# Kernel optimization log

Measured on AMD Instinct MI355X. Metric: run time of the kernel, lower is better.

## Reference

```python
import jax, jax.numpy as jnp
import numpy as np
from functools import partial

H = 51  # hidden size hard-coded in the module
B = 1024
T = 1024


def setup_inputs() -> dict:
    key = jax.random.key(0)
    ks = jax.random.split(key, 12)
    scale = 1.0 / np.sqrt(H)
    p = lambda k, shape: (jax.random.normal(k, shape, dtype=jnp.float32) * scale)
    return {
        "input": jax.random.normal(ks[0], (B, T), dtype=jnp.float32),
        # layer 1: LSTMCell(1, 51)
        "W_ih1": p(ks[1], (4 * H, 1)),
        "W_hh1": p(ks[2], (4 * H, H)),
        "b_ih1": p(ks[3], (4 * H,)),
        "b_hh1": p(ks[4], (4 * H,)),
        # layer 2: LSTMCell(51, 51)
        "W_ih2": p(ks[5], (4 * H, H)),
        "W_hh2": p(ks[6], (4 * H, H)),
        "b_ih2": p(ks[7], (4 * H,)),
        "b_hh2": p(ks[8], (4 * H,)),
        # Linear(51, 1)
        "W_lin": p(ks[9], (1, H)),
        "b_lin": p(ks[10], (1,)),
    }


def _lstm_cell(x, h, c, W_ih, W_hh, b_ih, b_hh):
    # PyTorch LSTMCell gate order: i, f, g, o
    gates = x @ W_ih.T + h @ W_hh.T + b_ih + b_hh  # [B, 4H]
    i, f, g, o = jnp.split(gates, 4, axis=-1)
    i = jax.nn.sigmoid(i)
    f = jax.nn.sigmoid(f)
    g = jnp.tanh(g)
    o = jax.nn.sigmoid(o)
    c_new = f * c + i * g
    h_new = o * jnp.tanh(c_new)
    return h_new, c_new


def reference(input, W_ih1, W_hh1, b_ih1, b_hh1, W_ih2, W_hh2, b_ih2, b_hh2, W_lin, b_lin):
    Bv = input.shape[0]
    dt = input.dtype
    init = (
        jnp.zeros((Bv, H), dt),  # h1
        jnp.zeros((Bv, H), dt),  # c1
        jnp.zeros((Bv, H), dt),  # h2
        jnp.zeros((Bv, H), dt),  # c2
    )

    def step(carry, x_t):  # x_t: [B, 1]
        h1, c1, h2, c2 = carry
        h1, c1 = _lstm_cell(x_t, h1, c1, W_ih1, W_hh1, b_ih1, b_hh1)
        h2, c2 = _lstm_cell(h1, h2, c2, W_ih2, W_hh2, b_ih2, b_hh2)
        y = h2 @ W_lin.T + b_lin  # [B, 1]
        return (h1, c1, h2, c2), y[:, 0]

    xs = input.T[:, :, None]  # [T, B, 1]
    _, ys = jax.lax.scan(step, init, xs)  # ys: [T, B]
    return ys.T  # [B, T]
```

## Files before the change

### kernel.cpp

```cpp
#include <hip/hip_runtime.h>


#define H     51
#define NROW  204
#define TLEN  1024
#define BPB   16
#define NTHR  896
#define NBLK  64
#define KPAD  88

#define LOG2E  1.442695041f
#define LOG2E2 2.885390082f

typedef __attribute__((ext_vector_type(8))) _Float16 half8;
typedef __attribute__((ext_vector_type(4))) float f4;

__device__ __forceinline__ float frcp(float x) { return __builtin_amdgcn_rcpf(x); }
#if __has_builtin(__builtin_amdgcn_exp2f)
__device__ __forceinline__ float ex2(float x) { return __builtin_amdgcn_exp2f(x); }
#else
__device__ __forceinline__ float ex2(float x) { return __expf(x * 0.6931471806f); }
#endif

__device__ __forceinline__ int posu(int u) {
    return (u & ~7) | ((u & 3) << 1) | ((u >> 2) & 1);
}
__device__ __forceinline__ int ipos(int p) {
    return (p & ~7) | ((p & 1) << 2) | ((p >> 1) & 3);
}

__device__ __forceinline__ half8 lds8h(const _Float16* p) {
    return *(const half8*)__builtin_assume_aligned(p, 16);
}

__device__ __forceinline__ void block_sync_lds() {
    asm volatile("s_waitcnt lgkmcnt(0)\n\ts_barrier" ::: "memory");
}

#define MFMA(ACC, A, B) \
    ACC = __builtin_amdgcn_mfma_f32_16x16x32_f16((A), (B), (ACC), 0, 0, 0)

__device__ __forceinline__ half8 load_wfrag(const float* __restrict__ W,
                                            int tile, int kt, int q, int mcol)
{
    half8 hf;
    const int prow = tile * 16 + mcol;
    const float sc = ((prow & 3) == 2) ? LOG2E2 : LOG2E;
#pragma unroll
    for (int j = 0; j < 8; ++j) {
        const int kk = ipos(kt * 32 + q * 8 + j);
        float v = 0.0f;
        if (prow < NROW && kk < H) {
            const int srow = (prow & 3) * H + (prow >> 2);
            v = W[srow * H + kk];
        }
        hf[j] = (_Float16)(v * sc);
    }
    return hf;
}

__device__ __forceinline__ float cell(float a_i, float a_f, float b_g,
                                      float d_o, float* c)
{
    const float e_i = ex2(-a_i);
    const float e_f = ex2(-a_f);
    const float Eg  = ex2(b_g);
    const float f   = frcp(1.0f + e_f);
    const float ig  = (Eg - 1.0f) * frcp((1.0f + e_i) * (Eg + 1.0f));
    const float cn  = fmaf(f, *c, ig);
    *c = cn;
    const float Ec  = ex2(cn * LOG2E2);
    const float e_o = ex2(-d_o);
    return (Ec - 1.0f) * frcp((Ec + 1.0f) * (1.0f + e_o));
}

__global__
__attribute__((amdgpu_flat_work_group_size(NTHR, NTHR), amdgpu_waves_per_eu(4, 4)))
void lstm2_kernel(const float* __restrict__ input,
                  const float* __restrict__ W_ih1, const float* __restrict__ W_hh1,
                  const float* __restrict__ b_ih1, const float* __restrict__ b_hh1,
                  const float* __restrict__ W_ih2, const float* __restrict__ W_hh2,
                  const float* __restrict__ b_ih2, const float* __restrict__ b_hh2,
                  const float* __restrict__ W_lin, const float* __restrict__ b_lin,
                  float* __restrict__ out)
{
    const int tid  = threadIdx.x;
    const int w    = tid >> 6;
    const int lane = tid & 63;
    const int q    = lane >> 4;
    const int mcol = lane & 15;
    const int b0   = blockIdx.x * BPB;

    const bool tile_wave = (w < 13);
    const bool y_wave    = (w == 13);

    __shared__ __align__(16) _Float16 hb[2][2][BPB][KPAD];

    {
        _Float16* hz = &hb[0][0][0][0];
        for (int i = tid; i < 2 * 2 * BPB * KPAD; i += NTHR) hz[i] = (_Float16)0.0f;
    }

    half8 A1[2], Ai[2], Ah[2];
    f4 bb1, bb2, wxv;
    float c1 = 0.0f, c2 = 0.0f;
    const int t = w;
    const int u = 4 * t + q;
    const int wpos = posu(u);

    if (tile_wave) {
#pragma unroll
        for (int kt = 0; kt < 2; ++kt) {
            A1[kt] = load_wfrag(W_hh1, t, kt, q, mcol);
            Ai[kt] = load_wfrag(W_ih2, t, kt, q, mcol);
            Ah[kt] = load_wfrag(W_hh2, t, kt, q, mcol);
        }
#pragma unroll
        for (int j = 0; j < 4; ++j) {
            const bool v = (u < H);
            const float sc = (j == 2) ? LOG2E2 : LOG2E;
            bb1[j] = v ? sc * (b_ih1[j * H + u] + b_hh1[j * H + u]) : 0.0f;
            bb2[j] = v ? sc * (b_ih2[j * H + u] + b_hh2[j * H + u]) : 0.0f;
            wxv[j] = v ? sc * W_ih1[j * H + u] : 0.0f;
        }
    }

    float wl[16];
    if (y_wave) {
#pragma unroll
        for (int i = 0; i < 16; ++i) {
            const int r = ipos(q * 16 + i);
            wl[i] = (r < H) ? W_lin[r] : 0.0f;
        }
    }
    const float blin = b_lin[0];

    float xcur = input[(size_t)(b0 + mcol) * TLEN + 0];

    __syncthreads();

#define STEP(KK, RB, WB, L2EN, YEN)                                            \
do {                                                                           \
    const int k_  = (KK);                                                      \
    const int kn_ = (k_ + 1 < TLEN) ? (k_ + 1) : (TLEN - 1);                   \
    const float xnext_ = input[(size_t)(b0 + mcol) * TLEN + kn_];              \
    if (tile_wave) {                                                           \
        half8 B1a = lds8h(&hb[RB][0][mcol][q * 8]);                            \
        half8 B1b = lds8h(&hb[RB][0][mcol][32 + q * 8]);                       \
        f4 g1;                                                                 \
        g1[0] = fmaf(wxv[0], xcur, bb1[0]);                                    \
        g1[1] = fmaf(wxv[1], xcur, bb1[1]);                                    \
        g1[2] = fmaf(wxv[2], xcur, bb1[2]);                                    \
        g1[3] = fmaf(wxv[3], xcur, bb1[3]);                                    \
        MFMA(g1, A1[0], B1a);  MFMA(g1, A1[1], B1b);                           \
                                                         \
        const float h1n = cell(g1[0], g1[1], g1[2], g1[3], &c1);               \
        hb[WB][0][mcol][wpos] = (_Float16)h1n;                                 \
        if (L2EN) {                                                            \
            half8 B2a = lds8h(&hb[RB][1][mcol][q * 8]);                        \
            half8 B2b = lds8h(&hb[RB][1][mcol][32 + q * 8]);                   \
            f4 g2 = bb2;                                                       \
            MFMA(g2, Ai[0], B1a);  MFMA(g2, Ai[1], B1b);                       \
            MFMA(g2, Ah[0], B2a);  MFMA(g2, Ah[1], B2b);                       \
                                                       \
            const float h2n = cell(g2[0], g2[1], g2[2], g2[3], &c2);           \
            hb[WB][1][mcol][wpos] = (_Float16)h2n;                             \
        }                                                                      \
    } else if (y_wave && (YEN)) {                                              \
               \
        half8 y0 = lds8h(&hb[RB][1][mcol][q * 16]);                            \
        half8 y1 = lds8h(&hb[RB][1][mcol][q * 16 + 8]);                        \
        float yp = 0.0f;                                                       \
        _Pragma("unroll")                                                      \
        for (int i = 0; i < 8; ++i) {                                          \
            yp += wl[i]     * (float)y0[i];                                    \
            yp += wl[i + 8] * (float)y1[i];                                    \
        }                                                                      \
        yp += __shfl_xor(yp, 16);                                              \
        yp += __shfl_xor(yp, 32);                                              \
        if (q == 0) out[(size_t)(b0 + mcol) * TLEN + (k_ - 2)] = yp + blin;    \
    }                                                                          \
    block_sync_lds();                                                          \
    xcur = xnext_;                                                             \
} while (0)

    STEP(0, 1, 0, 0, 0);
    STEP(1, 0, 1, 1, 0);
    for (int k = 2; k < TLEN; k += 2) {
        STEP(k, 1, 0, 1, 1);
        STEP(k + 1, 0, 1, 1, 1);
    }
    STEP(TLEN, 1, 0, 1, 1);
#undef STEP

    if (y_wave) {
        half8 y0 = lds8h(&hb[0][1][mcol][q * 16]);
        half8 y1 = lds8h(&hb[0][1][mcol][q * 16 + 8]);
        float yp = 0.0f;
#pragma unroll
        for (int i = 0; i < 8; ++i) {
            yp += wl[i]     * (float)y0[i];
            yp += wl[i + 8] * (float)y1[i];
        }
        yp += __shfl_xor(yp, 16);
        yp += __shfl_xor(yp, 32);
        if (q == 0) out[(size_t)(b0 + mcol) * TLEN + (TLEN - 1)] = yp + blin;
    }
}

extern "C" void kernel_launch(void* const* d_in, const int* in_sizes, int n_in,
                              void* d_out, int out_size, void* d_ws, size_t ws_size,
                              hipStream_t stream)
{
    const float* input = (const float*)d_in[0];
    const float* W_ih1 = (const float*)d_in[1];
    const float* W_hh1 = (const float*)d_in[2];
    const float* b_ih1 = (const float*)d_in[3];
    const float* b_hh1 = (const float*)d_in[4];
    const float* W_ih2 = (const float*)d_in[5];
    const float* W_hh2 = (const float*)d_in[6];
    const float* b_ih2 = (const float*)d_in[7];
    const float* b_hh2 = (const float*)d_in[8];
    const float* W_lin = (const float*)d_in[9];
    const float* b_lin = (const float*)d_in[10];

    float* out = (float*)d_out;

    hipLaunchKernelGGL(lstm2_kernel, dim3(NBLK), dim3(NTHR), 0, stream,
                       input, W_ih1, W_hh1, b_ih1, b_hh1,
                       W_ih2, W_hh2, b_ih2, b_hh2, W_lin, b_lin,
                       out);
}
```

Baseline: 772.0 us.

## Split LSTM layers across wave groups and pipeline layer 2 one step behind

Waves are re-partitioned so 7 waves compute layer 1 and 7 compute layer 2, with each wave owning two gate tiles. Layer 2 uses h1 prefetched into registers from the previous step, so the two layers run concurrently on different timesteps instead of serially inside one step. The separate output wave is removed and the linear projection is folded into a layer-2 wave that reuses the h2 fragments it already loaded. The change adds a four-deep h1 ring buffer, more registers per wave, a longer pipeline prologue and epilogue, and more complex index bookkeeping that could hide correctness errors.

```diff
diff --git a/kernel.cpp b/kernel.cpp
--- a/kernel.cpp
+++ b/kernel.cpp
@@ -91,116 +91,154 @@
     const int mcol = lane & 15;
     const int b0   = blockIdx.x * BPB;
 
-    const bool tile_wave = (w < 13);
-    const bool y_wave    = (w == 13);
-
-    __shared__ __align__(16) _Float16 hb[2][2][BPB][KPAD];
+    const bool isL1 = (w < 7);
+    const int  tw   = isL1 ? w : (w - 7);
+
+    __shared__ __align__(16) _Float16 h1r[4][BPB][KPAD];
+    __shared__ __align__(16) _Float16 h2r[2][BPB][KPAD];
 
     {
-        _Float16* hz = &hb[0][0][0][0];
-        for (int i = tid; i < 2 * 2 * BPB * KPAD; i += NTHR) hz[i] = (_Float16)0.0f;
-    }
-
-    half8 A1[2], Ai[2], Ah[2];
-    f4 bb1, bb2, wxv;
-    float c1 = 0.0f, c2 = 0.0f;
-    const int t = w;
-    const int u = 4 * t + q;
-    const int wpos = posu(u);
-
-    if (tile_wave) {
+        _Float16* p1 = &h1r[0][0][0];
+        for (int i = tid; i < 4 * BPB * KPAD; i += NTHR) p1[i] = (_Float16)0.0f;
+        _Float16* p2 = &h2r[0][0][0];
+        for (int i = tid; i < 2 * BPB * KPAD; i += NTHR) p2[i] = (_Float16)0.0f;
+    }
+
+    half8 Wa[2][2], Wb[2][2];
+    f4 bbv[2], wxv[2];
+    float cc[2] = {0.0f, 0.0f};
+    int wp[2];
+    const int tt[2] = {tw, 7 + tw};
+#pragma unroll
+    for (int s = 0; s < 2; ++s) {
+        const int t = tt[s];
+        const int u = 4 * t + q;
+        wp[s] = posu(u);
 #pragma unroll
         for (int kt = 0; kt < 2; ++kt) {
-            A1[kt] = load_wfrag(W_hh1, t, kt, q, mcol);
-            Ai[kt] = load_wfrag(W_ih2, t, kt, q, mcol);
-            Ah[kt] = load_wfrag(W_hh2, t, kt, q, mcol);
+            if (isL1) {
+                Wa[s][kt] = load_wfrag(W_hh1, t, kt, q, mcol);
+            } else {
+                Wa[s][kt] = load_wfrag(W_ih2, t, kt, q, mcol);
+                Wb[s][kt] = load_wfrag(W_hh2, t, kt, q, mcol);
+            }
         }
 #pragma unroll
         for (int j = 0; j < 4; ++j) {
-            const bool v = (u < H);
+            const bool v = (t < 13) && (u < H);
             const float sc = (j == 2) ? LOG2E2 : LOG2E;
-            bb1[j] = v ? sc * (b_ih1[j * H + u] + b_hh1[j * H + u]) : 0.0f;
-            bb2[j] = v ? sc * (b_ih2[j * H + u] + b_hh2[j * H + u]) : 0.0f;
-            wxv[j] = v ? sc * W_ih1[j * H + u] : 0.0f;
-        }
-    }
-
-    float wl[16];
-    if (y_wave) {
-#pragma unroll
-        for (int i = 0; i < 16; ++i) {
-            const int r = ipos(q * 16 + i);
-            wl[i] = (r < H) ? W_lin[r] : 0.0f;
+            if (isL1) {
+                bbv[s][j] = v ? sc * (b_ih1[j * H + u] + b_hh1[j * H + u]) : 0.0f;
+                wxv[s][j] = v ? sc * W_ih1[j * H + u] : 0.0f;
+            } else {
+                bbv[s][j] = v ? sc * (b_ih2[j * H + u] + b_hh2[j * H + u]) : 0.0f;
+                wxv[s][j] = 0.0f;
+            }
+        }
+    }
+
+    float wl_a[8], wl_b[8];
+    if (w == 7) {
+#pragma unroll
+        for (int j = 0; j < 8; ++j) {
+            const int ra = ipos(q * 8 + j);
+            const int rb = ipos(32 + q * 8 + j);
+            wl_a[j] = (ra < H) ? W_lin[ra] : 0.0f;
+            wl_b[j] = (rb < H) ? W_lin[rb] : 0.0f;
         }
     }
     const float blin = b_lin[0];
 
     float xcur = input[(size_t)(b0 + mcol) * TLEN + 0];
+    half8 e1a = {0, 0, 0, 0, 0, 0, 0, 0};
+    half8 e1b = {0, 0, 0, 0, 0, 0, 0, 0};
 
     __syncthreads();
 
-#define STEP(KK, RB, WB, L2EN, YEN)                                            \
+#define STEP(KK, S1W, S1R, S2W, S2R, L1E, L2E, YE, ERE)                        \
 do {                                                                           \
-    const int k_  = (KK);                                                      \
-    const int kn_ = (k_ + 1 < TLEN) ? (k_ + 1) : (TLEN - 1);                   \
-    const float xnext_ = input[(size_t)(b0 + mcol) * TLEN + kn_];              \
-    if (tile_wave) {                                                           \
-        half8 B1a = lds8h(&hb[RB][0][mcol][q * 8]);                            \
-        half8 B1b = lds8h(&hb[RB][0][mcol][32 + q * 8]);                       \
-        f4 g1;                                                                 \
-        g1[0] = fmaf(wxv[0], xcur, bb1[0]);                                    \
-        g1[1] = fmaf(wxv[1], xcur, bb1[1]);                                    \
-        g1[2] = fmaf(wxv[2], xcur, bb1[2]);                                    \
-        g1[3] = fmaf(wxv[3], xcur, bb1[3]);                                    \
-        MFMA(g1, A1[0], B1a);  MFMA(g1, A1[1], B1b);                           \
-                                                         \
-        const float h1n = cell(g1[0], g1[1], g1[2], g1[3], &c1);               \
-        hb[WB][0][mcol][wpos] = (_Float16)h1n;                                 \
-        if (L2EN) {                                                            \
-            half8 B2a = lds8h(&hb[RB][1][mcol][q * 8]);                        \
-            half8 B2b = lds8h(&hb[RB][1][mcol][32 + q * 8]);                   \
-            f4 g2 = bb2;                                                       \
-            MFMA(g2, Ai[0], B1a);  MFMA(g2, Ai[1], B1b);                       \
-            MFMA(g2, Ah[0], B2a);  MFMA(g2, Ah[1], B2b);                       \
-                                                       \
-            const float h2n = cell(g2[0], g2[1], g2[2], g2[3], &c2);           \
-            hb[WB][1][mcol][wpos] = (_Float16)h2n;                             \
+    const int k_ = (KK);                                                       \
+    if (isL1) {                                                                \
+        if (L1E) {                                                             \
+            const int kn_ = (k_ + 1 < TLEN) ? (k_ + 1) : (TLEN - 1);           \
+            const float xn_ = input[(size_t)(b0 + mcol) * TLEN + kn_];         \
+            half8 B1a = lds8h(&h1r[S1R][mcol][q * 8]);                         \
+            half8 B1b = lds8h(&h1r[S1R][mcol][32 + q * 8]);                    \
+            f4 g0, g1;                                                         \
+            g0[0] = fmaf(wxv[0][0], xcur, bbv[0][0]);                          \
+            g0[1] = fmaf(wxv[0][1], xcur, bbv[0][1]);                          \
+            g0[2] = fmaf(wxv[0][2], xcur, bbv[0][2]);                          \
+            g0[3] = fmaf(wxv[0][3], xcur, bbv[0][3]);                          \
+            g1[0] = fmaf(wxv[1][0], xcur, bbv[1][0]);                          \
+            g1[1] = fmaf(wxv[1][1], xcur, bbv[1][1]);                          \
+            g1[2] = fmaf(wxv[1][2], xcur, bbv[1][2]);                          \
+            g1[3] = fmaf(wxv[1][3], xcur, bbv[1][3]);                          \
+            MFMA(g0, Wa[0][0], B1a);  MFMA(g0, Wa[0][1], B1b);                 \
+            MFMA(g1, Wa[1][0], B1a);  MFMA(g1, Wa[1][1], B1b);                 \
+            const float h0 = cell(g0[0], g0[1], g0[2], g0[3], &cc[0]);         \
+            const float h1v = cell(g1[0], g1[1], g1[2], g1[3], &cc[1]);        \
+            h1r[S1W][mcol][wp[0]] = (_Float16)h0;                              \
+            h1r[S1W][mcol][wp[1]] = (_Float16)h1v;                             \
+            xcur = xn_;                                                        \
         }                                                                      \
-    } else if (y_wave && (YEN)) {                                              \
-               \
-        half8 y0 = lds8h(&hb[RB][1][mcol][q * 16]);                            \
-        half8 y1 = lds8h(&hb[RB][1][mcol][q * 16 + 8]);                        \
-        float yp = 0.0f;                                                       \
-        _Pragma("unroll")                                                      \
-        for (int i = 0; i < 8; ++i) {                                          \
-            yp += wl[i]     * (float)y0[i];                                    \
-            yp += wl[i + 8] * (float)y1[i];                                    \
+    } else {                                                                   \
+        if (L2E) {                                                             \
+            half8 B2a = lds8h(&h2r[S2R][mcol][q * 8]);                         \
+            half8 B2b = lds8h(&h2r[S2R][mcol][32 + q * 8]);                    \
+            f4 g0 = bbv[0], g1 = bbv[1];                                       \
+            MFMA(g0, Wa[0][0], e1a);  MFMA(g0, Wa[0][1], e1b);      \
+            MFMA(g1, Wa[1][0], e1a);  MFMA(g1, Wa[1][1], e1b);                 \
+            MFMA(g0, Wb[0][0], B2a);  MFMA(g0, Wb[0][1], B2b);                 \
+            MFMA(g1, Wb[1][0], B2a);  MFMA(g1, Wb[1][1], B2b);                 \
+            if (ERE) {             \
+                e1a = lds8h(&h1r[S1R][mcol][q * 8]);                           \
+                e1b = lds8h(&h1r[S1R][mcol][32 + q * 8]);                      \
+            }                                                                  \
+            const float h0 = cell(g0[0], g0[1], g0[2], g0[3], &cc[0]);         \
+            const float h1v = cell(g1[0], g1[1], g1[2], g1[3], &cc[1]);        \
+            h2r[S2W][mcol][wp[0]] = (_Float16)h0;                              \
+            h2r[S2W][mcol][wp[1]] = (_Float16)h1v;                             \
+            if ((YE) && w == 7) {    \
+                float yp = 0.0f;                                               \
+                _Pragma("unroll")                                              \
+                for (int j = 0; j < 8; ++j) {                                  \
+                    yp += wl_a[j] * (float)B2a[j];                             \
+                    yp += wl_b[j] * (float)B2b[j];                             \
+                }                                                              \
+                yp += __shfl_xor(yp, 16);                                      \
+                yp += __shfl_xor(yp, 32);                                      \
+                if (q == 0) out[(size_t)(b0 + mcol) * TLEN + (k_ - 3)] = yp + blin; \
+            }                                                                  \
+        } else if (ERE) {                                                      \
+            e1a = lds8h(&h1r[S1R][mcol][q * 8]);                               \
+            e1b = lds8h(&h1r[S1R][mcol][32 + q * 8]);                          \
         }                                                                      \
-        yp += __shfl_xor(yp, 16);                                              \
-        yp += __shfl_xor(yp, 32);                                              \
-        if (q == 0) out[(size_t)(b0 + mcol) * TLEN + (k_ - 2)] = yp + blin;    \
     }                                                                          \
     block_sync_lds();                                                          \
-    xcur = xnext_;                                                             \
 } while (0)
 
-    STEP(0, 1, 0, 0, 0);
-    STEP(1, 0, 1, 1, 0);
-    for (int k = 2; k < TLEN; k += 2) {
-        STEP(k, 1, 0, 1, 1);
-        STEP(k + 1, 0, 1, 1, 1);
-    }
-    STEP(TLEN, 1, 0, 1, 1);
+    STEP(0, 0, 3, 0, 1, 1, 0, 0, 0);
+    STEP(1, 1, 0, 1, 0, 1, 0, 0, 1);
+    STEP(2, 2, 1, 0, 1, 1, 1, 0, 1);
+    STEP(3, 3, 2, 1, 0, 1, 1, 1, 1);
+    for (int k = 4; k <= 1020; k += 4) {
+        STEP(k + 0, 0, 3, 0, 1, 1, 1, 1, 1);
+        STEP(k + 1, 1, 0, 1, 0, 1, 1, 1, 1);
+        STEP(k + 2, 2, 1, 0, 1, 1, 1, 1, 1);
+        STEP(k + 3, 3, 2, 1, 0, 1, 1, 1, 1);
+    }
+    STEP(1024, 0, 3, 0, 1, 0, 1, 1, 1);
+    STEP(1025, 1, 0, 1, 0, 0, 1, 1, 0);
 #undef STEP
 
-    if (y_wave) {
-        half8 y0 = lds8h(&hb[0][1][mcol][q * 16]);
-        half8 y1 = lds8h(&hb[0][1][mcol][q * 16 + 8]);
+    if (w == 7) {
+        half8 ya = lds8h(&h2r[1][mcol][q * 8]);
+        half8 yb = lds8h(&h2r[1][mcol][32 + q * 8]);
         float yp = 0.0f;
 #pragma unroll
-        for (int i = 0; i < 8; ++i) {
-            yp += wl[i]     * (float)y0[i];
-            yp += wl[i + 8] * (float)y1[i];
+        for (int j = 0; j < 8; ++j) {
+            yp += wl_a[j] * (float)ya[j];
+            yp += wl_b[j] * (float)yb[j];
         }
         yp += __shfl_xor(yp, 16);
         yp += __shfl_xor(yp, 32);
```

After: 724.2 us. 6.2% less time.
